# Kernel tuning notes

Hardware: AMD Instinct MI355X
Metric: run time of the kernel (lower is better)

The kernel has to match this reference:

```python
import jax, jax.numpy as jnp
import numpy as np

T, B, D, H = 512, 64, 1024, 1024

def setup_inputs() -> dict:
    key = jax.random.key(0)
    k1, k2, k3, k4 = jax.random.split(key, 4)
    s_x = 1.0 / np.sqrt(D)
    s_h = 1.0 / np.sqrt(H)
    return {
        "x": jax.random.normal(k1, (T, B, D), dtype=jnp.float32),
        "Wx": jax.random.uniform(k2, (4 * H, D), dtype=jnp.float32, minval=-s_x, maxval=s_x),
        "Wh": jax.random.uniform(k3, (4 * H, H), dtype=jnp.float32, minval=-s_h, maxval=s_h),
        "bh": jax.random.uniform(k4, (4 * H,), dtype=jnp.float32, minval=-s_h, maxval=s_h),
    }

def reference(x, Wx, Wh, bh):
    hdim = Wh.shape[1]
    bsz = x.shape[1]
    # Precompute input projection for all timesteps (same math as per-step W_x(x_t)).
    xg = jnp.einsum('tbd,gd->tbg', x, Wx)  # [T, B, 4H]

    def step(carry, xg_t):
        h, c = carry
        gates = xg_t + h @ Wh.T + bh  # [B, 4H]
        i, f, g, o = jnp.split(gates, 4, axis=-1)
        i = jax.nn.sigmoid(i)
        f = jax.nn.sigmoid(f)
        g = jnp.tanh(g)
        o = jax.nn.sigmoid(o)
        c = f * c + i * g
        h = o * jnp.tanh(c)
        return (h, c), h

    h0 = jnp.zeros((bsz, hdim), dtype=x.dtype)
    c0 = jnp.zeros((bsz, hdim), dtype=x.dtype)
    (h, c), outputs = jax.lax.scan(step, (h0, c0), xg)
    return outputs, h, c
```

## Files before the change

kernel.cpp:

```cpp
#include <hip/hip_runtime.h>
#include <cstddef>
#include <cstdint>


#define T_DIM 512
#define B_DIM 64
#define H_DIM 1024
#define G_DIM 4096
#define NBLK 256
#define BAR_STRIDE 16

typedef short short8 __attribute__((ext_vector_type(8)));
typedef float f32x4 __attribute__((ext_vector_type(4)));
typedef unsigned short ushort_t;
typedef unsigned long long u64_t;

__device__ __forceinline__ ushort_t f2b(float f) {
  union { float f; unsigned u; } v; v.f = f;
  unsigned r = v.u + 0x7fffu + ((v.u >> 16) & 1u);
  return (ushort_t)(r >> 16);
}
__device__ __forceinline__ float b2f(ushort_t u) {
  union { unsigned u; float f; } v; v.u = ((unsigned)u) << 16;
  return v.f;
}
__device__ __forceinline__ float sigmoidf_(float x) { return 1.0f / (1.0f + __expf(-x)); }

__device__ __forceinline__ void gload_lds16(const ushort_t* g, ushort_t* l) {
  __builtin_amdgcn_global_load_lds(
      (const __attribute__((address_space(1))) unsigned int*)g,
      (__attribute__((address_space(3))) unsigned int*)l, 16, 0, 0);
}

__global__ __launch_bounds__(256) void reset_flags_kernel(int* __restrict__ flg) {
  int i = blockIdx.x * 256 + threadIdx.x;
  if (i < NBLK * 4 * BAR_STRIDE) flg[i] = 0;
}

__global__ __launch_bounds__(256) void convert_bf16_kernel(
    const float* __restrict__ src, ushort_t* __restrict__ dst, int n8) {
  int i = blockIdx.x * 256 + threadIdx.x;
  if (i >= n8) return;
  float4 v0 = *(const float4*)&src[(size_t)i * 8];
  float4 v1 = *(const float4*)&src[(size_t)i * 8 + 4];
  ushort_t p[8] = {f2b(v0.x), f2b(v0.y), f2b(v0.z), f2b(v0.w),
                   f2b(v1.x), f2b(v1.y), f2b(v1.z), f2b(v1.w)};
  *(short8*)&dst[(size_t)i * 8] = *(const short8*)p;
}

__global__ __launch_bounds__(256) void xg_gemm_lds(
    const ushort_t* __restrict__ Ab, const ushort_t* __restrict__ Bb,
    const float* __restrict__ bh, ushort_t* __restrict__ C) {
  __shared__ ushort_t As[128 * 64];
  __shared__ ushort_t Bs[128 * 64];
  const int tid = threadIdx.x;
  const int lane = tid & 63;
  const int w = tid >> 6;
  const int wm = w >> 1, wn = w & 1;
  const int flat = (int)blockIdx.x;
  const int swz = (flat & 7) * 1024 + (flat >> 3);
  const size_t m0 = (size_t)(swz & 255) * 128;
  const int n0 = (swz >> 8) * 128;
  const int lr = lane & 15;
  const int lk = (lane >> 4) * 8;
  const int srow = lane >> 3;
  const int schk = lane & 7;

  f32x4 acc[4][4];
#pragma unroll
  for (int i = 0; i < 4; ++i)
#pragma unroll
    for (int j = 0; j < 4; ++j) acc[i][j] = 0.0f;

  for (int k0 = 0; k0 < 1024; k0 += 64) {
    __syncthreads();
#pragma unroll
    for (int i = 0; i < 4; ++i) {
      const int base_row = w * 32 + i * 8;
      const int row = base_row + srow;
      const int csrc = (schk ^ (row & 7)) * 8;
      gload_lds16(&Ab[(m0 + row) * 1024 + k0 + csrc], &As[base_row * 64]);
      gload_lds16(&Bb[(size_t)(n0 + row) * 1024 + k0 + csrc], &Bs[base_row * 64]);
    }
    __syncthreads();
#pragma unroll
    for (int kk = 0; kk < 64; kk += 32) {
      short8 af[4], bf[4];
#pragma unroll
      for (int mf = 0; mf < 4; ++mf) {
        const int row = wm * 64 + mf * 16 + lr;
        const int byte = (row * 128 + (kk + lk) * 2) ^ ((row & 7) << 4);
        af[mf] = *(const short8*)((const char*)As + byte);
      }
#pragma unroll
      for (int nf = 0; nf < 4; ++nf) {
        const int row = wn * 64 + nf * 16 + lr;
        const int byte = (row * 128 + (kk + lk) * 2) ^ ((row & 7) << 4);
        bf[nf] = *(const short8*)((const char*)Bs + byte);
      }
#pragma unroll
      for (int mf = 0; mf < 4; ++mf)
#pragma unroll
        for (int nf = 0; nf < 4; ++nf)
          acc[mf][nf] = __builtin_amdgcn_mfma_f32_16x16x32_bf16(
              af[mf], bf[nf], acc[mf][nf], 0, 0, 0);
    }
  }
#pragma unroll
  for (int nf = 0; nf < 4; ++nf) {
    const int col = n0 + wn * 64 + nf * 16 + lr;
    const float bias = bh[col];
#pragma unroll
    for (int mf = 0; mf < 4; ++mf) {
      const size_t row0 = m0 + wm * 64 + mf * 16 + (lane >> 4) * 4;
#pragma unroll
      for (int rr = 0; rr < 4; ++rr)
        C[(row0 + rr) * 4096 + col] = f2b(acc[mf][nf][rr] + bias);
    }
  }
}

__global__ __launch_bounds__(256) void xg_gemm_mfma(
    const float* __restrict__ A, const float* __restrict__ Bw,
    const float* __restrict__ bh, ushort_t* __restrict__ C) {
  __shared__ ushort_t As[128 * 64];
  __shared__ ushort_t Bs[128 * 64];
  const int tid = threadIdx.x;
  const int lane = tid & 63;
  const int w = tid >> 6;
  const int wm = w >> 1, wn = w & 1;
  const size_t m0 = (size_t)blockIdx.x * 128;
  const int n0 = blockIdx.y * 128;
  const int r = tid >> 1;
  const int kb = (tid & 1) * 32;
  f32x4 acc[4][4];
#pragma unroll
  for (int i = 0; i < 4; ++i)
#pragma unroll
    for (int j = 0; j < 4; ++j) acc[i][j] = 0.0f;
  const int lr = lane & 15;
  const int lk = (lane >> 4) * 8;
  for (int k0 = 0; k0 < 1024; k0 += 64) {
    __syncthreads();
#pragma unroll
    for (int i = 0; i < 4; ++i) {
      const int kk = kb + i * 8;
      float4 a0 = *(const float4*)&A[(m0 + r) * 1024 + k0 + kk];
      float4 a1 = *(const float4*)&A[(m0 + r) * 1024 + k0 + kk + 4];
      ushort_t pa[8] = {f2b(a0.x), f2b(a0.y), f2b(a0.z), f2b(a0.w),
                        f2b(a1.x), f2b(a1.y), f2b(a1.z), f2b(a1.w)};
      float4 b0 = *(const float4*)&Bw[(size_t)(n0 + r) * 1024 + k0 + kk];
      float4 b1 = *(const float4*)&Bw[(size_t)(n0 + r) * 1024 + k0 + kk + 4];
      ushort_t pb[8] = {f2b(b0.x), f2b(b0.y), f2b(b0.z), f2b(b0.w),
                        f2b(b1.x), f2b(b1.y), f2b(b1.z), f2b(b1.w)};
      const int byte = (r * 128 + kk * 2) ^ ((r & 7) << 4);
      *(short8*)((char*)As + byte) = *(const short8*)pa;
      *(short8*)((char*)Bs + byte) = *(const short8*)pb;
    }
    __syncthreads();
#pragma unroll
    for (int kk = 0; kk < 64; kk += 32) {
      short8 af[4], bf[4];
#pragma unroll
      for (int mf = 0; mf < 4; ++mf) {
        const int row = wm * 64 + mf * 16 + lr;
        const int byte = (row * 128 + (kk + lk) * 2) ^ ((row & 7) << 4);
        af[mf] = *(const short8*)((const char*)As + byte);
      }
#pragma unroll
      for (int nf = 0; nf < 4; ++nf) {
        const int row = wn * 64 + nf * 16 + lr;
        const int byte = (row * 128 + (kk + lk) * 2) ^ ((row & 7) << 4);
        bf[nf] = *(const short8*)((const char*)Bs + byte);
      }
#pragma unroll
      for (int mf = 0; mf < 4; ++mf)
#pragma unroll
        for (int nf = 0; nf < 4; ++nf)
          acc[mf][nf] = __builtin_amdgcn_mfma_f32_16x16x32_bf16(
              af[mf], bf[nf], acc[mf][nf], 0, 0, 0);
    }
  }
#pragma unroll
  for (int nf = 0; nf < 4; ++nf) {
    const int col = n0 + wn * 64 + nf * 16 + lr;
    const float bias = bh[col];
#pragma unroll
    for (int mf = 0; mf < 4; ++mf) {
      const size_t row0 = m0 + wm * 64 + mf * 16 + (lane >> 4) * 4;
#pragma unroll
      for (int rr = 0; rr < 4; ++rr)
        C[(row0 + rr) * 4096 + col] = f2b(acc[mf][nf][rr] + bias);
    }
  }
}

__global__ __launch_bounds__(256) void lstm_persistent(
    const ushort_t* __restrict__ xg,
    const ushort_t* __restrict__ Whb,
    ushort_t* __restrict__ hb0,
    ushort_t* __restrict__ hb1,
    int* __restrict__ flg,
    float* __restrict__ out) {
  extern __shared__ char smem[];
  ushort_t* Wlds = (ushort_t*)smem;
  float* accs = (float*)(smem + 131072);
  const int tid = threadIdx.x;
  const int lane = tid & 63;
  const int v = tid >> 6;
  const int bid = (int)blockIdx.x;
  const int j0 = (bid >> 2) * 16;
  const int w  = bid & 3;
  const int lr = lane & 15;
  const int lq = lane >> 4;

  const int bmine = w * 16 + v * 4 + lq;
  const int jmine = j0 + lr;
  const int* fpoll =
      &flg[((((16 * v + (lane >> 2)) * 4 + w) << 2) + (lane & 3)) * BAR_STRIDE];
  int* fmine = &flg[((bid << 2) + v) * BAR_STRIDE];

  for (int e = tid; e < 8192; e += 256) {
    const int r  = e >> 7;
    const int ch = e & 127;
    const int gr = (r >> 4) * 1024 + j0 + (r & 15);
    short8 val = *(const short8*)(Whb + (size_t)gr * 1024 + ch * 8);
    const int byte = (r * 2048 + ch * 16) ^ ((r & 7) << 4);
    *(short8*)((char*)Wlds + byte) = val;
  }
  __syncthreads();

  float creg = 0.f;
  float hv = 0.f;

  for (int t = 0; t < T_DIM; ++t) {
    const size_t xbase = ((size_t)t * 64 + bmine) * 4096 + jmine;
    float xgv[4];
#pragma unroll
    for (int g = 0; g < 4; ++g) xgv[g] = b2f(xg[xbase + (size_t)g * 1024]);

    f32x4 acc[4];
#pragma unroll
    for (int g = 0; g < 4; ++g) acc[g] = 0.f;

    if (t > 0) {
      int fv;
      do {
        fv = __hip_atomic_load(fpoll, __ATOMIC_RELAXED,
                               __HIP_MEMORY_SCOPE_AGENT);
      } while (!__all(fv >= t));
      asm volatile("" ::: "memory");

      const ushort_t* hprev = (t & 1) ? hb0 : hb1;
      const u64_t* hrow = (const u64_t*)(
          hprev + (size_t)(w * 16 + lr) * 1024 + v * 256 + lq * 8);
      short8 af[8];
#pragma unroll
      for (int i = 0; i < 8; ++i) {
        union { u64_t u[2]; short8 s; } av;
        av.u[0] = __hip_atomic_load(hrow + i * 8, __ATOMIC_RELAXED,
                                    __HIP_MEMORY_SCOPE_AGENT);
        av.u[1] = __hip_atomic_load(hrow + i * 8 + 1, __ATOMIC_RELAXED,
                                    __HIP_MEMORY_SCOPE_AGENT);
        af[i] = av.s;
      }
#pragma unroll
      for (int i = 0; i < 8; ++i) {
        const int ksg = v * 8 + i;
#pragma unroll
        for (int g = 0; g < 4; ++g) {
          const int row = g * 16 + lr;
          const int byte = (row * 2048 + ksg * 64 + lq * 16) ^ ((row & 7) << 4);
          short8 bfrag = *(const short8*)((const char*)Wlds + byte);
          acc[g] = __builtin_amdgcn_mfma_f32_16x16x32_bf16(af[i], bfrag,
                                                           acc[g], 0, 0, 0);
        }
      }
    }

#pragma unroll
    for (int g = 0; g < 4; ++g)
      *(f32x4*)&accs[((v * 4 + g) * 64 + lane) * 4] = acc[g];
    __syncthreads();

    float gv[4];
#pragma unroll
    for (int g = 0; g < 4; ++g) {
      float s = xgv[g];
#pragma unroll
      for (int v2 = 0; v2 < 4; ++v2)
        s += accs[((v2 * 4 + g) * 64 + v * 16 + lr) * 4 + lq];
      gv[g] = s;
    }
    const float ig = sigmoidf_(gv[0]);
    const float fg = sigmoidf_(gv[1]);
    const float gg = tanhf(gv[2]);
    const float og = sigmoidf_(gv[3]);
    const float cn = fmaf(fg, creg, ig * gg);
    creg = cn;
    hv = og * tanhf(cn);

    ushort_t* hcur = (t & 1) ? hb1 : hb0;
    __hip_atomic_store(&hcur[(size_t)bmine * 1024 + jmine], f2b(hv),
                       __ATOMIC_RELAXED, __HIP_MEMORY_SCOPE_AGENT);
    asm volatile("s_waitcnt vmcnt(0)" ::: "memory");
    if (t < T_DIM - 1 && lane == 0)
      __hip_atomic_store(fmine, t + 1, __ATOMIC_RELAXED,
                         __HIP_MEMORY_SCOPE_AGENT);

    __syncthreads();

    out[((size_t)t * 64 + bmine) * 1024 + jmine] = hv;
  }

  const size_t tail = (size_t)T_DIM * B_DIM * H_DIM;
  out[tail + (size_t)bmine * 1024 + jmine] = hv;
  out[tail + (size_t)B_DIM * H_DIM + (size_t)bmine * 1024 + jmine] = creg;
}

extern "C" void kernel_launch(void* const* d_in, const int* in_sizes, int n_in,
                              void* d_out, int out_size, void* d_ws, size_t ws_size,
                              hipStream_t stream) {
  const float* x  = (const float*)d_in[0];
  const float* Wx = (const float*)d_in[1];
  const float* Wh = (const float*)d_in[2];
  const float* bh = (const float*)d_in[3];
  float* out = (float*)d_out;

  const size_t xg_bytes  = (size_t)T_DIM * B_DIM * G_DIM * 2;
  const size_t wh_bytes  = (size_t)G_DIM * H_DIM * 2;
  const size_t hb_bytes  = (size_t)B_DIM * H_DIM * 2;
  const size_t flg_bytes = (size_t)NBLK * 4 * BAR_STRIDE * 4;
  const size_t x_bytes   = (size_t)T_DIM * B_DIM * H_DIM * 2;
  const size_t wx_bytes  = (size_t)G_DIM * H_DIM * 2;
  char* ws = (char*)d_ws;

  size_t off = 0;
  ushort_t* xg  = (ushort_t*)(ws + off); off += xg_bytes;
  ushort_t* Whb = (ushort_t*)(ws + off); off += wh_bytes;
  ushort_t* hb0 = (ushort_t*)(ws + off); off += hb_bytes;
  ushort_t* hb1 = (ushort_t*)(ws + off); off += hb_bytes;
  int*      flg = (int*)(ws + off);      off += flg_bytes;
  ushort_t* xb  = (ushort_t*)(ws + off); off += x_bytes;
  ushort_t* wxb = (ushort_t*)(ws + off); off += wx_bytes;
  const size_t need_full = off;

  reset_flags_kernel<<<(NBLK * 4 * BAR_STRIDE + 255) / 256, 256, 0, stream>>>(flg);
  convert_bf16_kernel<<<G_DIM * H_DIM / 8 / 256, 256, 0, stream>>>(
      Wh, Whb, G_DIM * H_DIM / 8);

  if (ws_size >= need_full) {
    convert_bf16_kernel<<<T_DIM * B_DIM * H_DIM / 8 / 256, 256, 0, stream>>>(
        x, xb, T_DIM * B_DIM * H_DIM / 8);
    convert_bf16_kernel<<<G_DIM * H_DIM / 8 / 256, 256, 0, stream>>>(
        Wx, wxb, G_DIM * H_DIM / 8);
    xg_gemm_lds<<<8192, 256, 0, stream>>>(xb, wxb, bh, xg);
  } else {
    xg_gemm_mfma<<<dim3(T_DIM * B_DIM / 128, G_DIM / 128), 256, 0, stream>>>(
        x, Wx, bh, xg);
  }
  lstm_persistent<<<NBLK, 256, 147456, stream>>>(xg, Whb, hb0, hb1, flg, out);
}
```

Baseline: 2.793 ms.

## Split each timestep into two half-batch phases with per-half flag barriers

The persistent LSTM loop now runs two sub-steps per timestep. Each sub-step handles half of each block's 16 batch rows, while the other half's MFMA inputs are zeroed. Flags are reorganized per (half, batch-group) slot with one flag per block written by thread 0 after a syncthreads. The intent is to pipeline across halves so one half's dependency wait overlaps the other half's compute, shortening the cross-block barrier critical path. The cost is double the loop iterations, redundant MFMAs on zero rows, and an extra barrier per sub-step.

```diff
diff --git a/kernel.cpp b/kernel.cpp
--- a/kernel.cpp
+++ b/kernel.cpp
@@ -9,6 +9,7 @@
 #define G_DIM 4096
 #define NBLK 256
 #define BAR_STRIDE 16
+#define FLG_SLOTS (2 * 4 * 64)
 
 typedef short short8 __attribute__((ext_vector_type(8)));
 typedef float f32x4 __attribute__((ext_vector_type(4)));
@@ -34,7 +35,7 @@
 
 __global__ __launch_bounds__(256) void reset_flags_kernel(int* __restrict__ flg) {
   int i = blockIdx.x * 256 + threadIdx.x;
-  if (i < NBLK * 4 * BAR_STRIDE) flg[i] = 0;
+  if (i < FLG_SLOTS * BAR_STRIDE) flg[i] = 0;
 }
 
 __global__ __launch_bounds__(256) void convert_bf16_kernel(
@@ -216,9 +217,7 @@
 
   const int bmine = w * 16 + v * 4 + lq;
   const int jmine = j0 + lr;
-  const int* fpoll =
-      &flg[((((16 * v + (lane >> 2)) * 4 + w) << 2) + (lane & 3)) * BAR_STRIDE];
-  int* fmine = &flg[((bid << 2) + v) * BAR_STRIDE];
+  const int myoct = v >> 1;
 
   for (int e = tid; e < 8192; e += 256) {
     const int r  = e >> 7;
@@ -233,36 +232,47 @@
   float creg = 0.f;
   float hv = 0.f;
 
-  for (int t = 0; t < T_DIM; ++t) {
-    const size_t xbase = ((size_t)t * 64 + bmine) * 4096 + jmine;
-    float xgv[4];
-#pragma unroll
-    for (int g = 0; g < 4; ++g) xgv[g] = b2f(xg[xbase + (size_t)g * 1024]);
+  for (int s = 0; s < 2 * T_DIM; ++s) {
+    const int t = s >> 1;
+    const int c = s & 1;
+    const bool own = (myoct == c);
+
+    float xgv[4] = {0.f, 0.f, 0.f, 0.f};
+    if (own) {
+      const size_t xbase = ((size_t)t * 64 + bmine) * 4096 + jmine;
+#pragma unroll
+      for (int g = 0; g < 4; ++g) xgv[g] = b2f(xg[xbase + (size_t)g * 1024]);
+    }
 
     f32x4 acc[4];
 #pragma unroll
     for (int g = 0; g < 4; ++g) acc[g] = 0.f;
 
     if (t > 0) {
+      const int* fp = &flg[(((c << 2) | w) * 64 + lane) * BAR_STRIDE];
       int fv;
       do {
-        fv = __hip_atomic_load(fpoll, __ATOMIC_RELAXED,
-                               __HIP_MEMORY_SCOPE_AGENT);
+        fv = __hip_atomic_load(fp, __ATOMIC_RELAXED, __HIP_MEMORY_SCOPE_AGENT);
       } while (!__all(fv >= t));
       asm volatile("" ::: "memory");
 
       const ushort_t* hprev = (t & 1) ? hb0 : hb1;
       const u64_t* hrow = (const u64_t*)(
           hprev + (size_t)(w * 16 + lr) * 1024 + v * 256 + lq * 8);
+      const bool vrow = ((lr >> 3) == c);
       short8 af[8];
 #pragma unroll
       for (int i = 0; i < 8; ++i) {
-        union { u64_t u[2]; short8 s; } av;
-        av.u[0] = __hip_atomic_load(hrow + i * 8, __ATOMIC_RELAXED,
-                                    __HIP_MEMORY_SCOPE_AGENT);
-        av.u[1] = __hip_atomic_load(hrow + i * 8 + 1, __ATOMIC_RELAXED,
-                                    __HIP_MEMORY_SCOPE_AGENT);
-        af[i] = av.s;
+        if (vrow) {
+          union { u64_t u[2]; short8 s8; } av;
+          av.u[0] = __hip_atomic_load(hrow + i * 8, __ATOMIC_RELAXED,
+                                      __HIP_MEMORY_SCOPE_AGENT);
+          av.u[1] = __hip_atomic_load(hrow + i * 8 + 1, __ATOMIC_RELAXED,
+                                      __HIP_MEMORY_SCOPE_AGENT);
+          af[i] = av.s8;
+        } else {
+          af[i] = short8{};
+        }
       }
 #pragma unroll
       for (int i = 0; i < 8; ++i) {
@@ -283,34 +293,36 @@
       *(f32x4*)&accs[((v * 4 + g) * 64 + lane) * 4] = acc[g];
     __syncthreads();
 
-    float gv[4];
-#pragma unroll
-    for (int g = 0; g < 4; ++g) {
-      float s = xgv[g];
-#pragma unroll
-      for (int v2 = 0; v2 < 4; ++v2)
-        s += accs[((v2 * 4 + g) * 64 + v * 16 + lr) * 4 + lq];
-      gv[g] = s;
-    }
-    const float ig = sigmoidf_(gv[0]);
-    const float fg = sigmoidf_(gv[1]);
-    const float gg = tanhf(gv[2]);
-    const float og = sigmoidf_(gv[3]);
-    const float cn = fmaf(fg, creg, ig * gg);
-    creg = cn;
-    hv = og * tanhf(cn);
-
-    ushort_t* hcur = (t & 1) ? hb1 : hb0;
-    __hip_atomic_store(&hcur[(size_t)bmine * 1024 + jmine], f2b(hv),
-                       __ATOMIC_RELAXED, __HIP_MEMORY_SCOPE_AGENT);
+    if (own) {
+      float gv[4];
+#pragma unroll
+      for (int g = 0; g < 4; ++g) {
+        float sum = xgv[g];
+#pragma unroll
+        for (int v2 = 0; v2 < 4; ++v2)
+          sum += accs[((v2 * 4 + g) * 64 + v * 16 + lr) * 4 + lq];
+        gv[g] = sum;
+      }
+      const float ig = sigmoidf_(gv[0]);
+      const float fg = sigmoidf_(gv[1]);
+      const float gg = tanhf(gv[2]);
+      const float og = sigmoidf_(gv[3]);
+      const float cn = fmaf(fg, creg, ig * gg);
+      creg = cn;
+      hv = og * tanhf(cn);
+      ushort_t* hcur = (t & 1) ? hb1 : hb0;
+      __hip_atomic_store(&hcur[(size_t)bmine * 1024 + jmine], f2b(hv),
+                         __ATOMIC_RELAXED, __HIP_MEMORY_SCOPE_AGENT);
+    }
+
     asm volatile("s_waitcnt vmcnt(0)" ::: "memory");
-    if (t < T_DIM - 1 && lane == 0)
-      __hip_atomic_store(fmine, t + 1, __ATOMIC_RELAXED,
-                         __HIP_MEMORY_SCOPE_AGENT);
-
-    __syncthreads();
-
-    out[((size_t)t * 64 + bmine) * 1024 + jmine] = hv;
+    __syncthreads();
+    if (t < T_DIM - 1 && tid == 0)
+      __hip_atomic_store(&flg[(((c << 2) | w) * 64 + (bid >> 2)) * BAR_STRIDE],
+                         t + 1, __ATOMIC_RELAXED, __HIP_MEMORY_SCOPE_AGENT);
+
+    if (own)
+      out[((size_t)t * 64 + bmine) * 1024 + jmine] = hv;
   }
 
   const size_t tail = (size_t)T_DIM * B_DIM * H_DIM;
@@ -330,7 +342,7 @@
   const size_t xg_bytes  = (size_t)T_DIM * B_DIM * G_DIM * 2;
   const size_t wh_bytes  = (size_t)G_DIM * H_DIM * 2;
   const size_t hb_bytes  = (size_t)B_DIM * H_DIM * 2;
-  const size_t flg_bytes = (size_t)NBLK * 4 * BAR_STRIDE * 4;
+  const size_t flg_bytes = (size_t)FLG_SLOTS * BAR_STRIDE * 4;
   const size_t x_bytes   = (size_t)T_DIM * B_DIM * H_DIM * 2;
   const size_t wx_bytes  = (size_t)G_DIM * H_DIM * 2;
   char* ws = (char*)d_ws;
@@ -345,7 +357,7 @@
   ushort_t* wxb = (ushort_t*)(ws + off); off += wx_bytes;
   const size_t need_full = off;
 
-  reset_flags_kernel<<<(NBLK * 4 * BAR_STRIDE + 255) / 256, 256, 0, stream>>>(flg);
+  reset_flags_kernel<<<(FLG_SLOTS * BAR_STRIDE + 255) / 256, 256, 0, stream>>>(flg);
   convert_bf16_kernel<<<G_DIM * H_DIM / 8 / 256, 256, 0, stream>>>(
       Wh, Whb, G_DIM * H_DIM / 8);
 
```

Result: slower. 4.480 ms (+60.4%).
